# Kernel optimization log

Hardware: AMD Instinct MI355X
Metric: run time of the kernel (lower is better)

The kernel has to match this reference:

```python
import jax, jax.numpy as jnp
import numpy as np

N, D, H = 50000, 256, 8
HD = D // H
E = 800000
NEG_SLOPE = 0.2


def setup_inputs() -> dict:
    key = jax.random.key(0)
    ks = jax.random.split(key, 12)
    s = 1.0 / np.sqrt(D)
    return {
        "x": jax.random.normal(ks[0], (N, D), jnp.float32),
        "edge_index": jax.random.randint(ks[1], (2, E), 0, N, jnp.int64),
        "edge_attr": jax.random.normal(ks[2], (E, 16), jnp.float32),
        # GATConv params: lin weight (no bias), attention vectors, output bias
        "W": jax.random.normal(ks[3], (D, D), jnp.float32) * s,
        "att_src": jax.random.normal(ks[4], (H, HD), jnp.float32) * s,
        "att_dst": jax.random.normal(ks[5], (H, HD), jnp.float32) * s,
        "bias": jnp.zeros((D,), jnp.float32),
        # LayerNorm
        "ln_g": jnp.ones((D,), jnp.float32),
        "ln_b": jnp.zeros((D,), jnp.float32),
        # FFN
        "W1": jax.random.normal(ks[6], (D, D), jnp.float32) * s,
        "b1": jnp.zeros((D,), jnp.float32),
        "W2": jax.random.normal(ks[7], (D, D), jnp.float32) * s,
        "b2": jnp.zeros((D,), jnp.float32),
    }


def _gat_layer(x, edge_index, W, att_src, att_dst, bias, ln_g, ln_b, W1, b1, W2, b2):
    n = x.shape[0]
    # GATConv default add_self_loops=True
    sl = jnp.arange(n, dtype=edge_index.dtype)
    src = jnp.concatenate([edge_index[0], sl])  # [E+N]
    dst = jnp.concatenate([edge_index[1], sl])  # [E+N]

    xp = (x @ W).reshape(n, H, HD)                      # [N,H,hd]
    a_src = jnp.einsum("nhd,hd->nh", xp, att_src)        # [N,H]
    a_dst = jnp.einsum("nhd,hd->nh", xp, att_dst)        # [N,H]

    e = a_src[src] + a_dst[dst]                          # [E+N,H]
    e = jax.nn.leaky_relu(e, NEG_SLOPE)
    # segment softmax over destination nodes (every node has a self loop)
    m = jax.ops.segment_max(e, dst, num_segments=n)      # [N,H]
    ex = jnp.exp(e - m[dst])
    denom = jax.ops.segment_sum(ex, dst, num_segments=n) # [N,H]
    alpha = ex / (denom[dst] + 1e-16)                    # [E+N,H]

    msg = alpha[:, :, None] * xp[src]                    # [E+N,H,hd]
    out = jax.ops.segment_sum(msg, dst, num_segments=n)  # [N,H,hd]
    h = out.reshape(n, D) + bias

    # residual + LayerNorm
    r = h + x
    mu = jnp.mean(r, axis=-1, keepdims=True)
    var = jnp.mean(jnp.square(r - mu), axis=-1, keepdims=True)
    hn = (r - mu) / jnp.sqrt(var + 1e-5) * ln_g + ln_b

    # FFN
    return jax.nn.relu(hn @ W1 + b1) @ W2 + b2


def reference(x, edge_index, edge_attr, W, att_src, att_dst, bias, ln_g, ln_b, W1, b1, W2, b2):
    # edge_attr is accepted but unused (GATConv built without edge_dim)
    return _gat_layer(x, edge_index, W, att_src, att_dst, bias, ln_g, ln_b, W1, b1, W2, b2)
```

## Files before the change

kernel.cpp:

```cpp
#include <hip/hip_runtime.h>
#include <hip/hip_bf16.h>

#define H 8
#define HD 32
#define DD 256
#define NEG_SLOPE 0.2f

typedef short bf16x8 __attribute__((ext_vector_type(8)));
typedef float f32x4 __attribute__((ext_vector_type(4)));

__device__ __forceinline__ unsigned short f2bf(float f) {
    unsigned int u = __float_as_uint(f);
    unsigned int r = (u + 0x7fffu + ((u >> 16) & 1u)) >> 16;
    return (unsigned short)r;
}
__device__ __forceinline__ float bf2f(unsigned short b) {
    return __uint_as_float(((unsigned int)b) << 16);
}

#define GLOAD_LDS16(g, s)                                                        \
    __builtin_amdgcn_global_load_lds((const __attribute__((address_space(1))) void*)(g), \
                                     (__attribute__((address_space(3))) void*)(s), 16, 0, 0)

__global__ __launch_bounds__(256) void prep(const float* __restrict__ x, unsigned short* __restrict__ xb,
                                            const float* __restrict__ W, unsigned short* __restrict__ Wt,
                                            const float* __restrict__ W1, unsigned short* __restrict__ W1t,
                                            const float* __restrict__ W2, unsigned short* __restrict__ W2t,
                                            int* __restrict__ cnt, int* __restrict__ fill,
                                            int N, int n4, int ZB) {
    int b = blockIdx.x;
    int tid = threadIdx.x;
    if (b < 768) {
        const float* src = (b < 256) ? W : (b < 512) ? W1 : W2;
        unsigned short* dst = (b < 256) ? Wt : (b < 512) ? W1t : W2t;
        int i = (b & 255) * 256 + tid;
        int n = i >> 8, k = i & 255;
        dst[i] = f2bf(src[k * 256 + n]);
    } else if (b < 768 + 2 * ZB) {
        int rb = b - 768;
        int* dst = (rb < ZB) ? cnt : fill;
        int i = (rb % ZB) * 256 + tid;
        if (i < N) dst[i] = 0;
    } else {
        int i = (b - 768 - 2 * ZB) * 256 + tid;
        if (i < n4) {
            float4 v = ((const float4*)x)[i];
            ushort4 o;
            o.x = f2bf(v.x); o.y = f2bf(v.y); o.z = f2bf(v.z); o.w = f2bf(v.w);
            ((ushort4*)xb)[i] = o;
        }
    }
}

enum { E_NONE = 0, E_BIAS_RELU = 1, E_BIAS = 2 };

template <int EPI, bool OBF, bool ATTN>
__global__ __launch_bounds__(256) void gemm_bf16(const unsigned short* __restrict__ A,
                                                 const unsigned short* __restrict__ Bt,
                                                 const float* __restrict__ bias,
                                                 void* __restrict__ Cout, int M,
                                                 const float* __restrict__ att_s,
                                                 const float* __restrict__ att_d,
                                                 float* __restrict__ a_srcO,
                                                 float* __restrict__ a_dstO) {
    constexpr int K = 256;
    __shared__ __align__(16) unsigned short Als[4096];
    __shared__ __align__(16) unsigned short Bls[4096];

    const int tid = threadIdx.x;
    const int l = tid & 63;
    const int w = tid >> 6;
    const int wr = w >> 1, wc = w & 1;
    const int row0 = blockIdx.x * 128;
    const int col0 = blockIdx.y * 128;

    const unsigned short* ga0 = A + (size_t)min(row0 + l, M - 1) * K + w * 8;
    const unsigned short* ga1 = A + (size_t)min(row0 + 64 + l, M - 1) * K + w * 8;
    const unsigned short* gb0 = Bt + (size_t)(col0 + l) * K + w * 8;
    const unsigned short* gb1 = Bt + (size_t)(col0 + 64 + l) * K + w * 8;
    unsigned short* la0 = &Als[(w * 128 + 0) * 8];
    unsigned short* la1 = &Als[(w * 128 + 64) * 8];
    unsigned short* lb0 = &Bls[(w * 128 + 0) * 8];
    unsigned short* lb1 = &Bls[(w * 128 + 64) * 8];

    const int q = l >> 4, r16 = l & 15;

    f32x4 zero = {0.f, 0.f, 0.f, 0.f};
    f32x4 acc[4][4];
#pragma unroll
    for (int i = 0; i < 4; i++)
#pragma unroll
        for (int j = 0; j < 4; j++) acc[i][j] = zero;

    for (int kk = 0; kk < K; kk += 32) {
        GLOAD_LDS16(ga0 + kk, la0);
        GLOAD_LDS16(ga1 + kk, la1);
        GLOAD_LDS16(gb0 + kk, lb0);
        GLOAD_LDS16(gb1 + kk, lb1);
        __syncthreads();
        bf16x8 af[4], bfr[4];
#pragma unroll
        for (int i = 0; i < 4; i++)
            af[i] = *(const bf16x8*)&Als[(q * 128 + wr * 64 + i * 16 + r16) * 8];
#pragma unroll
        for (int j = 0; j < 4; j++)
            bfr[j] = *(const bf16x8*)&Bls[(q * 128 + wc * 64 + j * 16 + r16) * 8];
#pragma unroll
        for (int i = 0; i < 4; i++)
#pragma unroll
            for (int j = 0; j < 4; j++)
                acc[i][j] = __builtin_amdgcn_mfma_f32_16x16x32_bf16(af[i], bfr[j], acc[i][j], 0, 0, 0);
        __syncthreads();
    }

    const int orow = row0 + wr * 64 + q * 4;
    const int ocol = col0 + wc * 64 + r16;

    float aws0, aws1, aws2, aws3, awd0, awd1, awd2, awd3;
    int hA = 0, hB = 0;
    if (ATTN) {
        hA = blockIdx.y * 4 + wc * 2;
        hB = hA + 1;
        aws0 = att_s[hA * HD + r16];
        aws1 = att_s[hA * HD + 16 + r16];
        aws2 = att_s[hB * HD + r16];
        aws3 = att_s[hB * HD + 16 + r16];
        awd0 = att_d[hA * HD + r16];
        awd1 = att_d[hA * HD + 16 + r16];
        awd2 = att_d[hB * HD + r16];
        awd3 = att_d[hB * HD + 16 + r16];
    }

#pragma unroll
    for (int i = 0; i < 4; i++) {
#pragma unroll
        for (int r = 0; r < 4; r++) {
            int row = orow + i * 16 + r;
            if (row < M) {
#pragma unroll
                for (int j = 0; j < 4; j++) {
                    int col = ocol + j * 16;
                    float v = acc[i][j][r];
                    if (EPI != E_NONE) v += bias[col];
                    if (EPI == E_BIAS_RELU) v = fmaxf(v, 0.f);
                    if (OBF)
                        ((unsigned short*)Cout)[(size_t)row * 256 + col] = f2bf(v);
                    else
                        ((float*)Cout)[(size_t)row * 256 + col] = v;
                }
            }
            if (ATTN) {
                float v0 = acc[i][0][r], v1 = acc[i][1][r];
                float v2 = acc[i][2][r], v3 = acc[i][3][r];
                float ps0 = v0 * aws0 + v1 * aws1;
                float ps1 = v2 * aws2 + v3 * aws3;
                float pd0 = v0 * awd0 + v1 * awd1;
                float pd1 = v2 * awd2 + v3 * awd3;
#pragma unroll
                for (int m = 1; m < 16; m <<= 1) {
                    ps0 += __shfl_xor(ps0, m, 64);
                    ps1 += __shfl_xor(ps1, m, 64);
                    pd0 += __shfl_xor(pd0, m, 64);
                    pd1 += __shfl_xor(pd1, m, 64);
                }
                if (r16 == 0 && row < M) {
                    a_srcO[row * H + hA] = ps0;
                    a_srcO[row * H + hB] = ps1;
                    a_dstO[row * H + hA] = pd0;
                    a_dstO[row * H + hB] = pd1;
                }
            }
        }
    }
}

__global__ void hist_kernel(const int* __restrict__ ei, int* __restrict__ counts, int E) {
    int e = blockIdx.x * blockDim.x + threadIdx.x;
    if (e < E) atomicAdd(&counts[ei[E + e]], 1);
}

__global__ __launch_bounds__(1024) void scan_block(const int* __restrict__ cnt,
                                                   int* __restrict__ row_ptr,
                                                   int* __restrict__ bsum, int N) {
    __shared__ int ws[16];
    int i = blockIdx.x * 1024 + threadIdx.x;
    int lane = threadIdx.x & 63, w = threadIdx.x >> 6;
    int v = (i < N) ? cnt[i] : 0;
    int sv = v;
#pragma unroll
    for (int off = 1; off < 64; off <<= 1) {
        int t = __shfl_up(sv, off, 64);
        if (lane >= off) sv += t;
    }
    if (lane == 63) ws[w] = sv;
    __syncthreads();
    if (w == 0) {
        int s = (lane < 16) ? ws[lane] : 0;
#pragma unroll
        for (int off = 1; off < 16; off <<= 1) {
            int t = __shfl_up(s, off, 64);
            if (lane >= off) s += t;
        }
        if (lane < 16) ws[lane] = s;
    }
    __syncthreads();
    int incl = sv + ((w > 0) ? ws[w - 1] : 0);
    if (i < N) row_ptr[i + 1] = incl;
    if (threadIdx.x == 1023) bsum[blockIdx.x] = incl;
}

__global__ void scan_partial(int* __restrict__ bsum, int nb) {
    int lane = threadIdx.x;
    int v = (lane < nb) ? bsum[lane] : 0;
    int s = v;
#pragma unroll
    for (int off = 1; off < 64; off <<= 1) {
        int t = __shfl_up(s, off, 64);
        if (lane >= off) s += t;
    }
    if (lane < nb) bsum[lane] = s - v;
}

__global__ __launch_bounds__(1024) void scan_add(int* __restrict__ row_ptr,
                                                 const int* __restrict__ bsum, int N) {
    int i = blockIdx.x * 1024 + threadIdx.x;
    if (i == 0) row_ptr[0] = 0;
    if (i < N) row_ptr[i + 1] += bsum[blockIdx.x];
}

__global__ void scatter_kernel(const int* __restrict__ ei, const int* __restrict__ row_ptr,
                               int* __restrict__ fill, int* __restrict__ src_sorted, int E) {
    int e = blockIdx.x * blockDim.x + threadIdx.x;
    if (e >= E) return;
    int s = ei[e];
    int d = ei[E + e];
    int pos = row_ptr[d] + atomicAdd(&fill[d], 1);
    src_sorted[pos] = s;
}

__global__ __launch_bounds__(256) void aggregate_ln(
    const unsigned short* __restrict__ xp, const float* __restrict__ x,
    const float* __restrict__ a_src, const float* __restrict__ a_dst,
    const int* __restrict__ row_ptr, const int* __restrict__ src_sorted,
    const float* __restrict__ bias, const float* __restrict__ ln_g,
    const float* __restrict__ ln_b, unsigned short* __restrict__ hn, int N) {
    int wave = threadIdx.x >> 6;
    int lane = threadIdx.x & 63;
    int n = blockIdx.x * 4 + wave;
    if (n >= N) return;
    int h = lane >> 3;

    float adst = a_dst[n * H + h];
    float e0 = a_src[n * H + h] + adst;
    e0 = (e0 > 0.f) ? e0 : NEG_SLOPE * e0;
    float ex = __expf(e0);
    ushort4 u = *(const ushort4*)(xp + (size_t)n * DD + lane * 4);
    float acc0 = ex * bf2f(u.x), acc1 = ex * bf2f(u.y);
    float acc2 = ex * bf2f(u.z), acc3 = ex * bf2f(u.w);
    float denom = ex;

    int beg = row_ptr[n], end = row_ptr[n + 1];
    int i = beg;
    for (; i + 3 < end; i += 4) {
        int s0 = src_sorted[i], s1 = src_sorted[i + 1];
        int s2 = src_sorted[i + 2], s3 = src_sorted[i + 3];
        float es0 = a_src[s0 * H + h], es1 = a_src[s1 * H + h];
        float es2 = a_src[s2 * H + h], es3 = a_src[s3 * H + h];
        ushort4 u0 = *(const ushort4*)(xp + (size_t)s0 * DD + lane * 4);
        ushort4 u1 = *(const ushort4*)(xp + (size_t)s1 * DD + lane * 4);
        ushort4 u2 = *(const ushort4*)(xp + (size_t)s2 * DD + lane * 4);
        ushort4 u3 = *(const ushort4*)(xp + (size_t)s3 * DD + lane * 4);
        float e0a = es0 + adst; e0a = (e0a > 0.f) ? e0a : NEG_SLOPE * e0a;
        float e1a = es1 + adst; e1a = (e1a > 0.f) ? e1a : NEG_SLOPE * e1a;
        float e2a = es2 + adst; e2a = (e2a > 0.f) ? e2a : NEG_SLOPE * e2a;
        float e3a = es3 + adst; e3a = (e3a > 0.f) ? e3a : NEG_SLOPE * e3a;
        float w0 = __expf(e0a), w1 = __expf(e1a);
        float w2 = __expf(e2a), w3 = __expf(e3a);
        acc0 += w0 * bf2f(u0.x) + w1 * bf2f(u1.x) + w2 * bf2f(u2.x) + w3 * bf2f(u3.x);
        acc1 += w0 * bf2f(u0.y) + w1 * bf2f(u1.y) + w2 * bf2f(u2.y) + w3 * bf2f(u3.y);
        acc2 += w0 * bf2f(u0.z) + w1 * bf2f(u1.z) + w2 * bf2f(u2.z) + w3 * bf2f(u3.z);
        acc3 += w0 * bf2f(u0.w) + w1 * bf2f(u1.w) + w2 * bf2f(u2.w) + w3 * bf2f(u3.w);
        denom += w0 + w1 + w2 + w3;
    }
    for (; i < end; i++) {
        int s0 = src_sorted[i];
        float es0 = a_src[s0 * H + h];
        ushort4 u0 = *(const ushort4*)(xp + (size_t)s0 * DD + lane * 4);
        float e0a = es0 + adst; e0a = (e0a > 0.f) ? e0a : NEG_SLOPE * e0a;
        float w0 = __expf(e0a);
        acc0 += w0 * bf2f(u0.x);
        acc1 += w0 * bf2f(u0.y);
        acc2 += w0 * bf2f(u0.z);
        acc3 += w0 * bf2f(u0.w);
        denom += w0;
    }
    float inv = 1.f / (denom + 1e-16f);
    float4 bb = *(const float4*)(bias + lane * 4);
    float4 xr = *(const float4*)(x + (size_t)n * DD + lane * 4);
    float r0 = acc0 * inv + bb.x + xr.x;
    float r1 = acc1 * inv + bb.y + xr.y;
    float r2 = acc2 * inv + bb.z + xr.z;
    float r3 = acc3 * inv + bb.w + xr.w;

    float s = r0 + r1 + r2 + r3;
#pragma unroll
    for (int m = 1; m < 64; m <<= 1) s += __shfl_xor(s, m, 64);
    float mu = s * (1.f / 256.f);
    float d0 = r0 - mu, d1 = r1 - mu, d2 = r2 - mu, d3 = r3 - mu;
    float qv = d0 * d0 + d1 * d1 + d2 * d2 + d3 * d3;
#pragma unroll
    for (int m = 1; m < 64; m <<= 1) qv += __shfl_xor(qv, m, 64);
    float rstd = rsqrtf(qv * (1.f / 256.f) + 1e-5f);
    float4 g = *(const float4*)(ln_g + lane * 4);
    float4 b = *(const float4*)(ln_b + lane * 4);
    ushort4 o;
    o.x = f2bf(d0 * rstd * g.x + b.x);
    o.y = f2bf(d1 * rstd * g.y + b.y);
    o.z = f2bf(d2 * rstd * g.z + b.z);
    o.w = f2bf(d3 * rstd * g.w + b.w);
    *(ushort4*)(hn + (size_t)n * DD + lane * 4) = o;
}

extern "C" void kernel_launch(void* const* d_in, const int* in_sizes, int n_in,
                              void* d_out, int out_size, void* d_ws, size_t ws_size,
                              hipStream_t stream) {
    const float* x = (const float*)d_in[0];
    const int* edge_index = (const int*)d_in[1];
    const float* W = (const float*)d_in[3];
    const float* att_src = (const float*)d_in[4];
    const float* att_dst = (const float*)d_in[5];
    const float* bias = (const float*)d_in[6];
    const float* ln_g = (const float*)d_in[7];
    const float* ln_b = (const float*)d_in[8];
    const float* W1 = (const float*)d_in[9];
    const float* b1 = (const float*)d_in[10];
    const float* W2 = (const float*)d_in[11];
    const float* b2 = (const float*)d_in[12];

    const int N = in_sizes[0] / DD;
    const int E = in_sizes[1] / 2;

    char* p = (char*)d_ws;
    auto carve = [&](size_t bytes) {
        char* r = p;
        p += (bytes + 255) & ~(size_t)255;
        return r;
    };
    unsigned short* x_bf = (unsigned short*)carve((size_t)N * DD * 2);
    unsigned short* xp_bf = (unsigned short*)carve((size_t)N * DD * 2);
    unsigned short* hn_bf = (unsigned short*)carve((size_t)N * DD * 2);
    float* a_src = (float*)carve((size_t)N * H * 4);
    float* a_dst = (float*)carve((size_t)N * H * 4);
    int* row_ptr = (int*)carve((size_t)(N + 1) * 4);
    int* cnt = (int*)carve((size_t)N * 4);
    int* fill = (int*)carve((size_t)N * 4);
    int* bsum = (int*)carve(256 * 4);
    int* src_sorted = (int*)carve((size_t)E * 4);
    unsigned short* Wt = (unsigned short*)carve(65536 * 2);
    unsigned short* W1t = (unsigned short*)carve(65536 * 2);
    unsigned short* W2t = (unsigned short*)carve(65536 * 2);
    unsigned short* t1_bf = x_bf;

    const int n4 = N * DD / 4;
    const int ZB = (N + 255) / 256;

    int prep_blocks = 768 + 2 * ZB + (n4 + 255) / 256;
    prep<<<prep_blocks, 256, 0, stream>>>(x, x_bf, W, Wt, W1, W1t, W2, W2t, cnt, fill, N, n4, ZB);

    dim3 ggrid((N + 127) / 128, 2);

    gemm_bf16<E_NONE, true, true><<<ggrid, 256, 0, stream>>>(
        x_bf, Wt, nullptr, xp_bf, N, att_src, att_dst, a_src, a_dst);

    hist_kernel<<<(E + 255) / 256, 256, 0, stream>>>(edge_index, cnt, E);
    int nb = (N + 1023) / 1024;
    scan_block<<<nb, 1024, 0, stream>>>(cnt, row_ptr, bsum, N);
    scan_partial<<<1, 64, 0, stream>>>(bsum, nb);
    scan_add<<<nb, 1024, 0, stream>>>(row_ptr, bsum, N);
    scatter_kernel<<<(E + 255) / 256, 256, 0, stream>>>(edge_index, row_ptr, fill, src_sorted, E);

    aggregate_ln<<<(N + 3) / 4, 256, 0, stream>>>(xp_bf, x, a_src, a_dst, row_ptr, src_sorted,
                                                  bias, ln_g, ln_b, hn_bf, N);

    gemm_bf16<E_BIAS_RELU, true, false><<<ggrid, 256, 0, stream>>>(
        hn_bf, W1t, b1, t1_bf, N, nullptr, nullptr, nullptr, nullptr);
    gemm_bf16<E_BIAS, false, false><<<ggrid, 256, 0, stream>>>(
        t1_bf, W2t, b2, d_out, N, nullptr, nullptr, nullptr, nullptr);
}
```

Baseline: 395.7 us.

## Fuse FFN GEMMs via LDS, widen GEMM tiles, simplify CSR scatter

The two FFN GEMMs become one kernel that keeps the ReLU intermediate in LDS. This removes the global write and read of t1. The GEMM tile changes to 64 rows by full 256 columns with K-step 64, so A is loaded once per row block. The CSR build drops the separate fill array and uses atomic increments on row_ptr, whose shifted values give the bounds the aggregate kernel reads. Aggregation unrolls to 8 edges and reads the residual from bf16 x, which adds rounding error to the residual.

```diff
diff --git a/kernel.cpp b/kernel.cpp
--- a/kernel.cpp
+++ b/kernel.cpp
@@ -26,8 +26,7 @@
                                             const float* __restrict__ W, unsigned short* __restrict__ Wt,
                                             const float* __restrict__ W1, unsigned short* __restrict__ W1t,
                                             const float* __restrict__ W2, unsigned short* __restrict__ W2t,
-                                            int* __restrict__ cnt, int* __restrict__ fill,
-                                            int N, int n4, int ZB) {
+                                            int* __restrict__ cnt, int N, int n4, int ZB) {
     int b = blockIdx.x;
     int tid = threadIdx.x;
     if (b < 768) {
@@ -36,13 +35,11 @@
         int i = (b & 255) * 256 + tid;
         int n = i >> 8, k = i & 255;
         dst[i] = f2bf(src[k * 256 + n]);
-    } else if (b < 768 + 2 * ZB) {
-        int rb = b - 768;
-        int* dst = (rb < ZB) ? cnt : fill;
-        int i = (rb % ZB) * 256 + tid;
-        if (i < N) dst[i] = 0;
+    } else if (b < 768 + ZB) {
+        int i = (b - 768) * 256 + tid;
+        if (i < N) cnt[i] = 0;
     } else {
-        int i = (b - 768 - 2 * ZB) * 256 + tid;
+        int i = (b - 768 - ZB) * 256 + tid;
         if (i < n4) {
             float4 v = ((const float4*)x)[i];
             ushort4 o;
@@ -52,38 +49,38 @@
     }
 }
 
-enum { E_NONE = 0, E_BIAS_RELU = 1, E_BIAS = 2 };
-
-template <int EPI, bool OBF, bool ATTN>
-__global__ __launch_bounds__(256) void gemm_bf16(const unsigned short* __restrict__ A,
-                                                 const unsigned short* __restrict__ Bt,
-                                                 const float* __restrict__ bias,
-                                                 void* __restrict__ Cout, int M,
-                                                 const float* __restrict__ att_s,
-                                                 const float* __restrict__ att_d,
-                                                 float* __restrict__ a_srcO,
-                                                 float* __restrict__ a_dstO) {
-    constexpr int K = 256;
+template <bool ATTN, bool PHASE2>
+__global__ __launch_bounds__(256) void gemm_fused(
+    const unsigned short* __restrict__ A,
+    const unsigned short* __restrict__ B1t, const float* __restrict__ b1,
+    const unsigned short* __restrict__ B2t, const float* __restrict__ b2,
+    void* __restrict__ Cout, int M,
+    const float* __restrict__ att_s, const float* __restrict__ att_d,
+    float* __restrict__ a_srcO, float* __restrict__ a_dstO) {
     __shared__ __align__(16) unsigned short Als[4096];
-    __shared__ __align__(16) unsigned short Bls[4096];
+    __shared__ __align__(16) unsigned short Bls[16384];
+    __shared__ __align__(16) unsigned short t1ls[PHASE2 ? 64 * 280 : 8];
 
     const int tid = threadIdx.x;
     const int l = tid & 63;
     const int w = tid >> 6;
-    const int wr = w >> 1, wc = w & 1;
-    const int row0 = blockIdx.x * 128;
-    const int col0 = blockIdx.y * 128;
-
-    const unsigned short* ga0 = A + (size_t)min(row0 + l, M - 1) * K + w * 8;
-    const unsigned short* ga1 = A + (size_t)min(row0 + 64 + l, M - 1) * K + w * 8;
-    const unsigned short* gb0 = Bt + (size_t)(col0 + l) * K + w * 8;
-    const unsigned short* gb1 = Bt + (size_t)(col0 + 64 + l) * K + w * 8;
-    unsigned short* la0 = &Als[(w * 128 + 0) * 8];
-    unsigned short* la1 = &Als[(w * 128 + 64) * 8];
-    unsigned short* lb0 = &Bls[(w * 128 + 0) * 8];
-    unsigned short* lb1 = &Bls[(w * 128 + 64) * 8];
-
-    const int q = l >> 4, r16 = l & 15;
+    const int r16 = l & 15, q0 = l >> 4;
+    const int row0 = blockIdx.x * 64;
+
+    const int ca0 = w * 128 + l, ca1 = ca0 + 64;
+    const unsigned short* gA0 = A + (size_t)min(row0 + (ca0 & 63), M - 1) * DD + (ca0 >> 6) * 8;
+    const unsigned short* gA1 = A + (size_t)min(row0 + (ca1 & 63), M - 1) * DD + (ca1 >> 6) * 8;
+    unsigned short* lA0 = &Als[ca0 * 8];
+    unsigned short* lA1 = &Als[ca1 * 8];
+
+    const unsigned short* gB[8];
+    unsigned short* lB[8];
+#pragma unroll
+    for (int k = 0; k < 8; k++) {
+        int c = w * 512 + k * 64 + l;
+        gB[k] = B1t + (size_t)(c & 255) * DD + (c >> 8) * 8;
+        lB[k] = &Bls[c * 8];
+    }
 
     f32x4 zero = {0.f, 0.f, 0.f, 0.f};
     f32x4 acc[4][4];
@@ -92,85 +89,147 @@
 #pragma unroll
         for (int j = 0; j < 4; j++) acc[i][j] = zero;
 
-    for (int kk = 0; kk < K; kk += 32) {
-        GLOAD_LDS16(ga0 + kk, la0);
-        GLOAD_LDS16(ga1 + kk, la1);
-        GLOAD_LDS16(gb0 + kk, lb0);
-        GLOAD_LDS16(gb1 + kk, lb1);
+    for (int kk = 0; kk < 256; kk += 64) {
+        GLOAD_LDS16(gA0 + kk, lA0);
+        GLOAD_LDS16(gA1 + kk, lA1);
+#pragma unroll
+        for (int k = 0; k < 8; k++) GLOAD_LDS16(gB[k] + kk, lB[k]);
         __syncthreads();
-        bf16x8 af[4], bfr[4];
-#pragma unroll
-        for (int i = 0; i < 4; i++)
-            af[i] = *(const bf16x8*)&Als[(q * 128 + wr * 64 + i * 16 + r16) * 8];
-#pragma unroll
-        for (int j = 0; j < 4; j++)
-            bfr[j] = *(const bf16x8*)&Bls[(q * 128 + wc * 64 + j * 16 + r16) * 8];
-#pragma unroll
-        for (int i = 0; i < 4; i++)
+#pragma unroll
+        for (int t = 0; t < 2; t++) {
+            int q = t * 4 + q0;
+            bf16x8 af[4], bf[4];
+#pragma unroll
+            for (int i = 0; i < 4; i++)
+                af[i] = *(const bf16x8*)&Als[(q * 64 + i * 16 + r16) * 8];
 #pragma unroll
             for (int j = 0; j < 4; j++)
-                acc[i][j] = __builtin_amdgcn_mfma_f32_16x16x32_bf16(af[i], bfr[j], acc[i][j], 0, 0, 0);
+                bf[j] = *(const bf16x8*)&Bls[(q * 256 + w * 64 + j * 16 + r16) * 8];
+#pragma unroll
+            for (int i = 0; i < 4; i++)
+#pragma unroll
+                for (int j = 0; j < 4; j++)
+                    acc[i][j] = __builtin_amdgcn_mfma_f32_16x16x32_bf16(af[i], bf[j], acc[i][j], 0, 0, 0);
+        }
         __syncthreads();
     }
 
-    const int orow = row0 + wr * 64 + q * 4;
-    const int ocol = col0 + wc * 64 + r16;
-
-    float aws0, aws1, aws2, aws3, awd0, awd1, awd2, awd3;
-    int hA = 0, hB = 0;
-    if (ATTN) {
-        hA = blockIdx.y * 4 + wc * 2;
-        hB = hA + 1;
-        aws0 = att_s[hA * HD + r16];
-        aws1 = att_s[hA * HD + 16 + r16];
-        aws2 = att_s[hB * HD + r16];
-        aws3 = att_s[hB * HD + 16 + r16];
-        awd0 = att_d[hA * HD + r16];
-        awd1 = att_d[hA * HD + 16 + r16];
-        awd2 = att_d[hB * HD + r16];
-        awd3 = att_d[hB * HD + 16 + r16];
-    }
-
-#pragma unroll
-    for (int i = 0; i < 4; i++) {
-#pragma unroll
-        for (int r = 0; r < 4; r++) {
-            int row = orow + i * 16 + r;
-            if (row < M) {
-#pragma unroll
-                for (int j = 0; j < 4; j++) {
-                    int col = ocol + j * 16;
-                    float v = acc[i][j][r];
-                    if (EPI != E_NONE) v += bias[col];
-                    if (EPI == E_BIAS_RELU) v = fmaxf(v, 0.f);
-                    if (OBF)
-                        ((unsigned short*)Cout)[(size_t)row * 256 + col] = f2bf(v);
-                    else
-                        ((float*)Cout)[(size_t)row * 256 + col] = v;
+    if (!PHASE2) {
+        float aws0, aws1, aws2, aws3, awd0, awd1, awd2, awd3;
+        int hA = 0, hB = 0;
+        if (ATTN) {
+            hA = w * 2; hB = hA + 1;
+            aws0 = att_s[hA * HD + r16];
+            aws1 = att_s[hA * HD + 16 + r16];
+            aws2 = att_s[hB * HD + r16];
+            aws3 = att_s[hB * HD + 16 + r16];
+            awd0 = att_d[hA * HD + r16];
+            awd1 = att_d[hA * HD + 16 + r16];
+            awd2 = att_d[hB * HD + r16];
+            awd3 = att_d[hB * HD + 16 + r16];
+        }
+#pragma unroll
+        for (int i = 0; i < 4; i++) {
+#pragma unroll
+            for (int r = 0; r < 4; r++) {
+                int row = row0 + i * 16 + q0 * 4 + r;
+                if (row < M) {
+#pragma unroll
+                    for (int j = 0; j < 4; j++) {
+                        int col = w * 64 + j * 16 + r16;
+                        ((unsigned short*)Cout)[(size_t)row * DD + col] = f2bf(acc[i][j][r]);
+                    }
+                }
+                if (ATTN) {
+                    float v0 = acc[i][0][r], v1 = acc[i][1][r];
+                    float v2 = acc[i][2][r], v3 = acc[i][3][r];
+                    float ps0 = v0 * aws0 + v1 * aws1;
+                    float ps1 = v2 * aws2 + v3 * aws3;
+                    float pd0 = v0 * awd0 + v1 * awd1;
+                    float pd1 = v2 * awd2 + v3 * awd3;
+#pragma unroll
+                    for (int m = 1; m < 16; m <<= 1) {
+                        ps0 += __shfl_xor(ps0, m, 64);
+                        ps1 += __shfl_xor(ps1, m, 64);
+                        pd0 += __shfl_xor(pd0, m, 64);
+                        pd1 += __shfl_xor(pd1, m, 64);
+                    }
+                    if (r16 == 0 && row < M) {
+                        a_srcO[row * H + hA] = ps0;
+                        a_srcO[row * H + hB] = ps1;
+                        a_dstO[row * H + hA] = pd0;
+                        a_dstO[row * H + hB] = pd1;
+                    }
                 }
             }
-            if (ATTN) {
-                float v0 = acc[i][0][r], v1 = acc[i][1][r];
-                float v2 = acc[i][2][r], v3 = acc[i][3][r];
-                float ps0 = v0 * aws0 + v1 * aws1;
-                float ps1 = v2 * aws2 + v3 * aws3;
-                float pd0 = v0 * awd0 + v1 * awd1;
-                float pd1 = v2 * awd2 + v3 * awd3;
-#pragma unroll
-                for (int m = 1; m < 16; m <<= 1) {
-                    ps0 += __shfl_xor(ps0, m, 64);
-                    ps1 += __shfl_xor(ps1, m, 64);
-                    pd0 += __shfl_xor(pd0, m, 64);
-                    pd1 += __shfl_xor(pd1, m, 64);
-                }
-                if (r16 == 0 && row < M) {
-                    a_srcO[row * H + hA] = ps0;
-                    a_srcO[row * H + hB] = ps1;
-                    a_dstO[row * H + hA] = pd0;
-                    a_dstO[row * H + hB] = pd1;
+        }
+    } else {
+        float bb1[4];
+#pragma unroll
+        for (int j = 0; j < 4; j++) bb1[j] = b1[w * 64 + j * 16 + r16];
+#pragma unroll
+        for (int i = 0; i < 4; i++)
+#pragma unroll
+            for (int r = 0; r < 4; r++) {
+                int rl = i * 16 + q0 * 4 + r;
+#pragma unroll
+                for (int j = 0; j < 4; j++) {
+                    float v = fmaxf(acc[i][j][r] + bb1[j], 0.f);
+                    t1ls[rl * 280 + w * 64 + j * 16 + r16] = f2bf(v);
                 }
             }
-        }
+        __syncthreads();
+
+        const unsigned short* gB2[8];
+#pragma unroll
+        for (int k = 0; k < 8; k++) {
+            int c = w * 512 + k * 64 + l;
+            gB2[k] = B2t + (size_t)(c & 255) * DD + (c >> 8) * 8;
+        }
+#pragma unroll
+        for (int i = 0; i < 4; i++)
+#pragma unroll
+            for (int j = 0; j < 4; j++) acc[i][j] = zero;
+
+        for (int kk = 0; kk < 256; kk += 64) {
+#pragma unroll
+            for (int k = 0; k < 8; k++) GLOAD_LDS16(gB2[k] + kk, lB[k]);
+            __syncthreads();
+#pragma unroll
+            for (int t = 0; t < 2; t++) {
+                int q = t * 4 + q0;
+                bf16x8 af[4], bf[4];
+#pragma unroll
+                for (int i = 0; i < 4; i++)
+                    af[i] = *(const bf16x8*)&t1ls[(i * 16 + r16) * 280 + kk + q * 8];
+#pragma unroll
+                for (int j = 0; j < 4; j++)
+                    bf[j] = *(const bf16x8*)&Bls[(q * 256 + w * 64 + j * 16 + r16) * 8];
+#pragma unroll
+                for (int i = 0; i < 4; i++)
+#pragma unroll
+                    for (int j = 0; j < 4; j++)
+                        acc[i][j] = __builtin_amdgcn_mfma_f32_16x16x32_bf16(af[i], bf[j], acc[i][j], 0, 0, 0);
+            }
+            __syncthreads();
+        }
+
+        float bb2[4];
+#pragma unroll
+        for (int j = 0; j < 4; j++) bb2[j] = b2[w * 64 + j * 16 + r16];
+#pragma unroll
+        for (int i = 0; i < 4; i++)
+#pragma unroll
+            for (int r = 0; r < 4; r++) {
+                int row = row0 + i * 16 + q0 * 4 + r;
+                if (row < M) {
+#pragma unroll
+                    for (int j = 0; j < 4; j++) {
+                        int col = w * 64 + j * 16 + r16;
+                        ((float*)Cout)[(size_t)row * DD + col] = acc[i][j][r] + bb2[j];
+                    }
+                }
+            }
     }
 }
 
@@ -228,20 +287,20 @@
     if (i < N) row_ptr[i + 1] += bsum[blockIdx.x];
 }
 
-__global__ void scatter_kernel(const int* __restrict__ ei, const int* __restrict__ row_ptr,
-                               int* __restrict__ fill, int* __restrict__ src_sorted, int E) {
+__global__ void scatter_kernel(const int* __restrict__ ei, int* __restrict__ row_ptr,
+                               int* __restrict__ src_sorted, int E) {
     int e = blockIdx.x * blockDim.x + threadIdx.x;
     if (e >= E) return;
     int s = ei[e];
     int d = ei[E + e];
-    int pos = row_ptr[d] + atomicAdd(&fill[d], 1);
+    int pos = atomicAdd(&row_ptr[d], 1);
     src_sorted[pos] = s;
 }
 
 __global__ __launch_bounds__(256) void aggregate_ln(
-    const unsigned short* __restrict__ xp, const float* __restrict__ x,
+    const unsigned short* __restrict__ xp, const unsigned short* __restrict__ x_bf,
     const float* __restrict__ a_src, const float* __restrict__ a_dst,
-    const int* __restrict__ row_ptr, const int* __restrict__ src_sorted,
+    const int* __restrict__ rp, const int* __restrict__ src_sorted,
     const float* __restrict__ bias, const float* __restrict__ ln_g,
     const float* __restrict__ ln_b, unsigned short* __restrict__ hn, int N) {
     int wave = threadIdx.x >> 6;
@@ -259,34 +318,37 @@
     float acc2 = ex * bf2f(u.z), acc3 = ex * bf2f(u.w);
     float denom = ex;
 
-    int beg = row_ptr[n], end = row_ptr[n + 1];
+    int beg = (n > 0) ? rp[n - 1] : 0;
+    int end = rp[n];
     int i = beg;
-    for (; i + 3 < end; i += 4) {
-        int s0 = src_sorted[i], s1 = src_sorted[i + 1];
-        int s2 = src_sorted[i + 2], s3 = src_sorted[i + 3];
-        float es0 = a_src[s0 * H + h], es1 = a_src[s1 * H + h];
-        float es2 = a_src[s2 * H + h], es3 = a_src[s3 * H + h];
-        ushort4 u0 = *(const ushort4*)(xp + (size_t)s0 * DD + lane * 4);
-        ushort4 u1 = *(const ushort4*)(xp + (size_t)s1 * DD + lane * 4);
-        ushort4 u2 = *(const ushort4*)(xp + (size_t)s2 * DD + lane * 4);
-        ushort4 u3 = *(const ushort4*)(xp + (size_t)s3 * DD + lane * 4);
-        float e0a = es0 + adst; e0a = (e0a > 0.f) ? e0a : NEG_SLOPE * e0a;
-        float e1a = es1 + adst; e1a = (e1a > 0.f) ? e1a : NEG_SLOPE * e1a;
-        float e2a = es2 + adst; e2a = (e2a > 0.f) ? e2a : NEG_SLOPE * e2a;
-        float e3a = es3 + adst; e3a = (e3a > 0.f) ? e3a : NEG_SLOPE * e3a;
-        float w0 = __expf(e0a), w1 = __expf(e1a);
-        float w2 = __expf(e2a), w3 = __expf(e3a);
-        acc0 += w0 * bf2f(u0.x) + w1 * bf2f(u1.x) + w2 * bf2f(u2.x) + w3 * bf2f(u3.x);
-        acc1 += w0 * bf2f(u0.y) + w1 * bf2f(u1.y) + w2 * bf2f(u2.y) + w3 * bf2f(u3.y);
-        acc2 += w0 * bf2f(u0.z) + w1 * bf2f(u1.z) + w2 * bf2f(u2.z) + w3 * bf2f(u3.z);
-        acc3 += w0 * bf2f(u0.w) + w1 * bf2f(u1.w) + w2 * bf2f(u2.w) + w3 * bf2f(u3.w);
-        denom += w0 + w1 + w2 + w3;
+    for (; i + 7 < end; i += 8) {
+        int s[8];
+        float es[8];
+        ushort4 uu[8];
+#pragma unroll
+        for (int k = 0; k < 8; k++) s[k] = src_sorted[i + k];
+#pragma unroll
+        for (int k = 0; k < 8; k++) es[k] = a_src[s[k] * H + h];
+#pragma unroll
+        for (int k = 0; k < 8; k++) uu[k] = *(const ushort4*)(xp + (size_t)s[k] * DD + lane * 4);
+#pragma unroll
+        for (int k = 0; k < 8; k++) {
+            float e = es[k] + adst;
+            e = (e > 0.f) ? e : NEG_SLOPE * e;
+            float wk = __expf(e);
+            acc0 += wk * bf2f(uu[k].x);
+            acc1 += wk * bf2f(uu[k].y);
+            acc2 += wk * bf2f(uu[k].z);
+            acc3 += wk * bf2f(uu[k].w);
+            denom += wk;
+        }
     }
     for (; i < end; i++) {
         int s0 = src_sorted[i];
         float es0 = a_src[s0 * H + h];
         ushort4 u0 = *(const ushort4*)(xp + (size_t)s0 * DD + lane * 4);
-        float e0a = es0 + adst; e0a = (e0a > 0.f) ? e0a : NEG_SLOPE * e0a;
+        float e0a = es0 + adst;
+        e0a = (e0a > 0.f) ? e0a : NEG_SLOPE * e0a;
         float w0 = __expf(e0a);
         acc0 += w0 * bf2f(u0.x);
         acc1 += w0 * bf2f(u0.y);
@@ -296,11 +358,11 @@
     }
     float inv = 1.f / (denom + 1e-16f);
     float4 bb = *(const float4*)(bias + lane * 4);
-    float4 xr = *(const float4*)(x + (size_t)n * DD + lane * 4);
-    float r0 = acc0 * inv + bb.x + xr.x;
-    float r1 = acc1 * inv + bb.y + xr.y;
-    float r2 = acc2 * inv + bb.z + xr.z;
-    float r3 = acc3 * inv + bb.w + xr.w;
+    ushort4 xr = *(const ushort4*)(x_bf + (size_t)n * DD + lane * 4);
+    float r0 = acc0 * inv + bb.x + bf2f(xr.x);
+    float r1 = acc1 * inv + bb.y + bf2f(xr.y);
+    float r2 = acc2 * inv + bb.z + bf2f(xr.z);
+    float r3 = acc3 * inv + bb.w + bf2f(xr.w);
 
     float s = r0 + r1 + r2 + r3;
 #pragma unroll
@@ -353,37 +415,33 @@
     float* a_dst = (float*)carve((size_t)N * H * 4);
     int* row_ptr = (int*)carve((size_t)(N + 1) * 4);
     int* cnt = (int*)carve((size_t)N * 4);
-    int* fill = (int*)carve((size_t)N * 4);
     int* bsum = (int*)carve(256 * 4);
     int* src_sorted = (int*)carve((size_t)E * 4);
     unsigned short* Wt = (unsigned short*)carve(65536 * 2);
     unsigned short* W1t = (unsigned short*)carve(65536 * 2);
     unsigned short* W2t = (unsigned short*)carve(65536 * 2);
-    unsigned short* t1_bf = x_bf;
 
     const int n4 = N * DD / 4;
     const int ZB = (N + 255) / 256;
 
-    int prep_blocks = 768 + 2 * ZB + (n4 + 255) / 256;
-    prep<<<prep_blocks, 256, 0, stream>>>(x, x_bf, W, Wt, W1, W1t, W2, W2t, cnt, fill, N, n4, ZB);
-
-    dim3 ggrid((N + 127) / 128, 2);
-
-    gemm_bf16<E_NONE, true, true><<<ggrid, 256, 0, stream>>>(
-        x_bf, Wt, nullptr, xp_bf, N, att_src, att_dst, a_src, a_dst);
+    int prep_blocks = 768 + ZB + (n4 + 255) / 256;
+    prep<<<prep_blocks, 256, 0, stream>>>(x, x_bf, W, Wt, W1, W1t, W2, W2t, cnt, N, n4, ZB);
+
+    const int gblocks = (N + 63) / 64;
+
+    gemm_fused<true, false><<<gblocks, 256, 0, stream>>>(
+        x_bf, Wt, nullptr, nullptr, nullptr, xp_bf, N, att_src, att_dst, a_src, a_dst);
 
     hist_kernel<<<(E + 255) / 256, 256, 0, stream>>>(edge_index, cnt, E);
     int nb = (N + 1023) / 1024;
     scan_block<<<nb, 1024, 0, stream>>>(cnt, row_ptr, bsum, N);
     scan_partial<<<1, 64, 0, stream>>>(bsum, nb);
     scan_add<<<nb, 1024, 0, stream>>>(row_ptr, bsum, N);
-    scatter_kernel<<<(E + 255) / 256, 256, 0, stream>>>(edge_index, row_ptr, fill, src_sorted, E);
-
-    aggregate_ln<<<(N + 3) / 4, 256, 0, stream>>>(xp_bf, x, a_src, a_dst, row_ptr, src_sorted,
+    scatter_kernel<<<(E + 255) / 256, 256, 0, stream>>>(edge_index, row_ptr, src_sorted, E);
+
+    aggregate_ln<<<(N + 3) / 4, 256, 0, stream>>>(xp_bf, x_bf, a_src, a_dst, row_ptr, src_sorted,
                                                   bias, ln_g, ln_b, hn_bf, N);
 
-    gemm_bf16<E_BIAS_RELU, true, false><<<ggrid, 256, 0, stream>>>(
-        hn_bf, W1t, b1, t1_bf, N, nullptr, nullptr, nullptr, nullptr);
-    gemm_bf16<E_BIAS, false, false><<<ggrid, 256, 0, stream>>>(
-        t1_bf, W2t, b2, d_out, N, nullptr, nullptr, nullptr, nullptr);
-}
+    gemm_fused<false, true><<<gblocks, 256, 0, stream>>>(
+        hn_bf, W1t, b1, W2t, b2, d_out, N, nullptr, nullptr, nullptr, nullptr);
+}
```

After: 390.3 us. About the same (-1.4%).
